# Optimization experiments

Measured on AMD Instinct MI355X. Metric: run time of the kernel, lower is better.

## Reference

```python
import jax, jax.numpy as jnp
import numpy as np

N = 50000      # nodes
E = 800000     # edges (before self-loops)
C_IN, C_H, C_OUT = 128, 64, 64
NEG_SLOPE = 0.2  # PyG GATConv default LeakyReLU slope


def setup_inputs() -> dict:
    key = jax.random.key(0)
    ks = jax.random.split(key, 16)
    def w(k, shape, fan_in):
        return jax.random.normal(k, shape, jnp.float32) / np.sqrt(fan_in)
    return {
        "x": jax.random.normal(ks[0], (N, C_IN), jnp.float32),
        "edge_index": jax.random.randint(ks[1], (2, E), 0, N, jnp.int32),
        "W1": w(ks[2], (C_IN, C_H), C_IN),
        "a_src1": w(ks[3], (C_H,), C_H),
        "a_dst1": w(ks[4], (C_H,), C_H),
        "b1": jnp.zeros((C_H,), jnp.float32),
        "W2": w(ks[5], (C_H, C_H), C_H),
        "a_src2": w(ks[6], (C_H,), C_H),
        "a_dst2": w(ks[7], (C_H,), C_H),
        "b2": jnp.zeros((C_H,), jnp.float32),
        "W3": w(ks[8], (C_H, C_OUT), C_H),
        "a_src3": w(ks[9], (C_OUT,), C_OUT),
        "a_dst3": w(ks[10], (C_OUT,), C_OUT),
        "b3": jnp.zeros((C_OUT,), jnp.float32),
    }


def _gat_conv(x, src, dst, W, a_src, a_dst, b):
    # Single-head GATConv (eval mode, self-loops already appended).
    h = x @ W                                   # [N, C]
    alpha_s = h @ a_src                         # [N]
    alpha_d = h @ a_dst                         # [N]
    e = jax.nn.leaky_relu(alpha_s[src] + alpha_d[dst], NEG_SLOPE)  # [E']
    # segment softmax over edges sharing the same destination node
    m = jax.lax.stop_gradient(jax.ops.segment_max(e, dst, num_segments=N))
    w = jnp.exp(e - m[dst])
    denom = jax.ops.segment_sum(w, dst, num_segments=N)
    alpha = w / denom[dst]                      # [E']
    out = jax.ops.segment_sum(h[src] * alpha[:, None], dst, num_segments=N)
    return out + b


def reference(x, edge_index, W1, a_src1, a_dst1, b1, W2, a_src2, a_dst2, b2,
              W3, a_src3, a_dst3, b3):
    loop = jnp.arange(N, dtype=edge_index.dtype)
    src = jnp.concatenate([edge_index[0], loop])  # add self-loops (PyG default)
    dst = jnp.concatenate([edge_index[1], loop])
    h = jax.nn.elu(_gat_conv(x, src, dst, W1, a_src1, a_dst1, b1))
    h = jax.nn.elu(_gat_conv(h, src, dst, W2, a_src2, a_dst2, b2))
    return _gat_conv(h, src, dst, W3, a_src3, a_dst3, b3)
```

## Files before the change

kernel.cpp:

```cpp
#include <hip/hip_runtime.h>
#include <hip/hip_bf16.h>
#include <math.h>

#define N_NODES 50000
#define N_EDGES 800000
#define ET_EDGES (N_EDGES + N_NODES)
#define NEG_SLOPE 0.2f
#define NBUCK ((N_NODES + 255) / 256)
#define CHUNK 4096
#define CAP   8192

typedef __hip_bfloat16 bf16;
typedef float f32x2 __attribute__((ext_vector_type(2)));

__device__ inline float bfbits(unsigned short u) {
    return __uint_as_float(((unsigned)u) << 16);
}
__device__ inline float bflo(unsigned u) { return __uint_as_float(u << 16); }
__device__ inline float bfhi(unsigned u) { return __uint_as_float(u & 0xffff0000u); }
__device__ inline f32x2 unpk(unsigned u) {
    f32x2 r; r.x = bflo(u); r.y = bfhi(u); return r;
}
__device__ inline f32x2 bcast2(float v) { f32x2 r; r.x = v; r.y = v; return r; }

struct PrepArgs {
    const void* src[12];
    float*      dst[12];
    int         n[12];
};

__global__ __launch_bounds__(256)
void prep(PrepArgs a, const unsigned short* __restrict__ w1raw,
          unsigned* __restrict__ flag, int* __restrict__ cur256)
{
    __shared__ unsigned sflag;
    const int tid = threadIdx.x;
    if (tid < 64) {
        float v0 = bfbits(w1raw[2 * tid]);
        float v1 = bfbits(w1raw[2 * tid + 1]);
        bool bad = !(fabsf(v0) <= 64.f && fabsf(v1) <= 64.f);
        unsigned long long b = __ballot(bad);
        if (tid == 0) sflag = (b == 0ull) ? 1u : 0u;
    }
    __syncthreads();
    const bool isbf = (sflag != 0u);
    const int which = blockIdx.y;

    if (which == 12) {
        int i = blockIdx.x * 256 + tid;
        if (i < NBUCK) cur256[i] = i * CAP;
        if (blockIdx.x == 0 && tid == 0) *flag = isbf ? 1u : 0u;
        return;
    }
    const int n = a.n[which];
    const void* s = a.src[which];
    float* d = a.dst[which];
    for (int i = blockIdx.x * 256 + tid; i < n; i += 8 * 256)
        d[i] = isbf ? bfbits(((const unsigned short*)s)[i])
                    : ((const float*)s)[i];
}

__global__ __launch_bounds__(256)
void binpass(const int* __restrict__ ei, int* __restrict__ cur256,
             unsigned* __restrict__ scratch)
{
    __shared__ int hist[NBUCK];
    __shared__ int lpre[NBUCK + 1];
    __shared__ int lcur[NBUCK];
    __shared__ int gbase[NBUCK];
    __shared__ int scan_a[256];
    __shared__ unsigned entry[CHUNK];

    const int tid = threadIdx.x;
    const int e0  = blockIdx.x * CHUNK;
    const int n   = min(CHUNK, ET_EDGES - e0);

    if (tid < NBUCK) hist[tid] = 0;
    __syncthreads();

    for (int k = tid; k < n; k += 256) {
        int e = e0 + k;
        int d = (e < N_EDGES) ? ei[N_EDGES + e] : e - N_EDGES;
        atomicAdd(&hist[d >> 8], 1);
    }
    __syncthreads();

    int v = (tid < NBUCK) ? hist[tid] : 0;
    scan_a[tid] = v;
    __syncthreads();
    for (int off = 1; off < 256; off <<= 1) {
        int t = (tid >= off) ? scan_a[tid - off] : 0;
        __syncthreads();
        scan_a[tid] += t;
        __syncthreads();
    }
    if (tid < NBUCK) lpre[tid] = scan_a[tid] - v;
    if (tid == NBUCK - 1) lpre[NBUCK] = scan_a[tid];
    if (tid < NBUCK) {
        gbase[tid] = v ? atomicAdd(&cur256[tid], v) : 0;
        lcur[tid] = 0;
    }
    __syncthreads();

    for (int k = tid; k < n; k += 256) {
        int e = e0 + k;
        int s, d;
        if (e < N_EDGES) { s = ei[e]; d = ei[N_EDGES + e]; }
        else             { s = d = e - N_EDGES; }
        int b = d >> 8;
        int p = atomicAdd(&lcur[b], 1);
        entry[lpre[b] + p] = ((unsigned)s << 8) | (unsigned)(d & 255);
    }
    __syncthreads();

    for (int i = tid; i < n; i += 256) {
        int lo = 0, hi = NBUCK;
        while (hi - lo > 1) {
            int mid = (lo + hi) >> 1;
            if (lpre[mid] <= i) lo = mid; else hi = mid;
        }
        scratch[gbase[lo] + (i - lpre[lo])] = entry[i];
    }
}

__global__ __launch_bounds__(256)
void fine_scatter(const int* __restrict__ cur256,
                  const unsigned* __restrict__ scratch,
                  int* __restrict__ csr_src,
                  int* __restrict__ rowptr)
{
    __shared__ int scnt[256];
    __shared__ int cnt[256];
    __shared__ int pre[256];
    const int tid = threadIdx.x;
    const int b   = blockIdx.x;
    const int nb  = b * 256;
    const int nn  = min(256, N_NODES - nb);

    int bv = (tid < NBUCK) ? (cur256[tid] - tid * CAP) : 0;
    scnt[tid] = bv;
    __syncthreads();
    for (int off = 1; off < 256; off <<= 1) {
        int u = (tid >= off) ? scnt[tid - off] : 0;
        __syncthreads();
        scnt[tid] += u;
        __syncthreads();
    }
    const int gb = scnt[b] - (cur256[b] - b * CAP);
    const int n  = cur256[b] - b * CAP;
    const long seg = (long)b * CAP;

    cnt[tid] = 0;
    __syncthreads();
    for (int i = tid; i < n; i += 256)
        atomicAdd(&cnt[scratch[seg + i] & 255u], 1);
    __syncthreads();

    int v = cnt[tid];
    pre[tid] = v;
    __syncthreads();
    for (int off = 1; off < 256; off <<= 1) {
        int t = (tid >= off) ? pre[tid - off] : 0;
        __syncthreads();
        pre[tid] += t;
        __syncthreads();
    }
    int excl = pre[tid] - v + gb;
    if (tid < nn) rowptr[nb + tid] = excl;
    if (b == NBUCK - 1 && tid == 0) rowptr[N_NODES] = ET_EDGES;
    cnt[tid] = excl;
    __syncthreads();

    for (int i = tid; i < n; i += 256) {
        unsigned e = scratch[seg + i];
        int p = atomicAdd(&cnt[e & 255u], 1);
        csr_src[p] = (int)(e >> 8);
    }
}

template<int CIN, int XMODE>
__global__ __launch_bounds__(256)
void gemm_alpha(const void* __restrict__ x,
                const float* __restrict__ W,
                const float* __restrict__ a_src,
                const float* __restrict__ a_dst,
                const unsigned* __restrict__ flag,
                bf16* __restrict__ hb,
                float* __restrict__ as_out,
                float* __restrict__ ad_out)
{
    constexpr int CINP = CIN + 4;
    __shared__ float sW[CIN * 64];
    __shared__ float sx[64 * CINP];
    const bool isbf = (XMODE == 2) || (XMODE == 1 && *flag != 0u);
    const int tid  = threadIdx.x;
    const int colg = tid & 15;
    const int rowg = tid >> 4;
    const int c0   = colg * 4;
    const int r0l  = rowg * 4;
    const int row0 = blockIdx.x * 64;

    for (int i = tid * 4; i < CIN * 64; i += 1024)
        *(float4*)&sW[i] = *(const float4*)&W[i];

    const long xbase = (long)row0 * CIN;
    const int  tile  = 64 * CIN;
    const int  limit = (N_NODES - row0) * CIN;
    if (isbf) {
        const unsigned short* xb = (const unsigned short*)x + xbase;
        for (int i = tid * 4; i < tile; i += 1024) {
            float4 v = {0.f, 0.f, 0.f, 0.f};
            if (i < limit) {
                ushort4 u = *(const ushort4*)&xb[i];
                v.x = bfbits(u.x); v.y = bfbits(u.y);
                v.z = bfbits(u.z); v.w = bfbits(u.w);
            }
            const int r = i / CIN, k = i & (CIN - 1);
            *(float4*)&sx[r * CINP + k] = v;
        }
    } else {
        const float* xf = (const float*)x + xbase;
        for (int i = tid * 4; i < tile; i += 1024) {
            float4 v = {0.f, 0.f, 0.f, 0.f};
            if (i < limit) v = *(const float4*)&xf[i];
            const int r = i / CIN, k = i & (CIN - 1);
            *(float4*)&sx[r * CINP + k] = v;
        }
    }
    __syncthreads();

    f32x2 acc[4][2];
#pragma unroll
    for (int r = 0; r < 4; ++r) {
        acc[r][0] = (f32x2){0.f, 0.f};
        acc[r][1] = (f32x2){0.f, 0.f};
    }

#pragma unroll 2
    for (int kk = 0; kk < CIN; kk += 4) {
        const float4 w0 = *(const float4*)&sW[(kk + 0) * 64 + c0];
        const float4 w1 = *(const float4*)&sW[(kk + 1) * 64 + c0];
        const float4 w2 = *(const float4*)&sW[(kk + 2) * 64 + c0];
        const float4 w3 = *(const float4*)&sW[(kk + 3) * 64 + c0];
        f32x2 w0lo; w0lo.x = w0.x; w0lo.y = w0.y;
        f32x2 w0hi; w0hi.x = w0.z; w0hi.y = w0.w;
        f32x2 w1lo; w1lo.x = w1.x; w1lo.y = w1.y;
        f32x2 w1hi; w1hi.x = w1.z; w1hi.y = w1.w;
        f32x2 w2lo; w2lo.x = w2.x; w2lo.y = w2.y;
        f32x2 w2hi; w2hi.x = w2.z; w2hi.y = w2.w;
        f32x2 w3lo; w3lo.x = w3.x; w3lo.y = w3.y;
        f32x2 w3hi; w3hi.x = w3.z; w3hi.y = w3.w;
#pragma unroll
        for (int r = 0; r < 4; ++r) {
            const float4 xv = *(const float4*)&sx[(r0l + r) * CINP + kk];
            acc[r][0] = __builtin_elementwise_fma(bcast2(xv.x), w0lo, acc[r][0]);
            acc[r][1] = __builtin_elementwise_fma(bcast2(xv.x), w0hi, acc[r][1]);
            acc[r][0] = __builtin_elementwise_fma(bcast2(xv.y), w1lo, acc[r][0]);
            acc[r][1] = __builtin_elementwise_fma(bcast2(xv.y), w1hi, acc[r][1]);
            acc[r][0] = __builtin_elementwise_fma(bcast2(xv.z), w2lo, acc[r][0]);
            acc[r][1] = __builtin_elementwise_fma(bcast2(xv.z), w2hi, acc[r][1]);
            acc[r][0] = __builtin_elementwise_fma(bcast2(xv.w), w3lo, acc[r][0]);
            acc[r][1] = __builtin_elementwise_fma(bcast2(xv.w), w3hi, acc[r][1]);
        }
    }

    const float4 sa4 = *(const float4*)&a_src[c0];
    const float4 sd4 = *(const float4*)&a_dst[c0];
#pragma unroll
    for (int r = 0; r < 4; ++r) {
        const int row = row0 + r0l + r;
        const float h0 = acc[r][0].x, h1 = acc[r][0].y;
        const float h2 = acc[r][1].x, h3 = acc[r][1].y;
        float vs = fmaf(h0, sa4.x, fmaf(h1, sa4.y, fmaf(h2, sa4.z, h3 * sa4.w)));
        float vd = fmaf(h0, sd4.x, fmaf(h1, sd4.y, fmaf(h2, sd4.z, h3 * sd4.w)));
#pragma unroll
        for (int off = 1; off < 16; off <<= 1) {
            vs += __shfl_xor(vs, off, 64);
            vd += __shfl_xor(vd, off, 64);
        }
        if (row < N_NODES) {
            uint2 u;
            u.x = ((unsigned)__bfloat16_as_ushort(__float2bfloat16(h0))) |
                  (((unsigned)__bfloat16_as_ushort(__float2bfloat16(h1))) << 16);
            u.y = ((unsigned)__bfloat16_as_ushort(__float2bfloat16(h2))) |
                  (((unsigned)__bfloat16_as_ushort(__float2bfloat16(h3))) << 16);
            *(uint2*)&((unsigned short*)hb)[(long)row * 64 + c0] = u;
            if (colg == 0) { as_out[row] = vs; ad_out[row] = vd; }
        }
    }
}

#define EDGE4_FMA(wX, pX) {                                                  \
    f32x2 w2_ = { wX, wX };                                                  \
    A0 = __builtin_elementwise_fma(w2_, unpk(pX.x), A0);                     \
    A1 = __builtin_elementwise_fma(w2_, unpk(pX.y), A1);                     \
    A2 = __builtin_elementwise_fma(w2_, unpk(pX.z), A2);                     \
    A3 = __builtin_elementwise_fma(w2_, unpk(pX.w), A3); }

template<bool DO_ELU, int OMODE>
__global__ __launch_bounds__(256)
void gat_gather(const int* __restrict__ rowptr,
                const int* __restrict__ csr_src,
                const float* __restrict__ as_in,
                const float* __restrict__ ad_in,
                const unsigned short* __restrict__ hb_in,
                const float* __restrict__ bias,
                void* __restrict__ out,
                const unsigned* __restrict__ flag)
{
    const int tid  = threadIdx.x;
    const int lane = tid & 63;
    const int l16  = lane & 15;
    const int gb16 = lane & 48;
    const int sub  = l16 >> 3;
    const int c8   = (l16 & 7) * 8;
    const int node = blockIdx.x * 16 + (tid >> 4);
    if (node >= N_NODES) return;

    const int beg = rowptr[node];
    const int deg = rowptr[node + 1] - beg;
    const float adv = ad_in[node];

    int   msrc0 = 0, msrc1 = 0;
    float mw0 = 0.f, mw1 = 0.f;
    if (l16 < deg) {
        msrc0 = csr_src[beg + l16];
        float v = as_in[msrc0] + adv;
        v = (v > 0.f) ? v : NEG_SLOPE * v;
        mw0 = __expf(fminf(v, 60.f));
    }
    if (16 + l16 < deg) {
        msrc1 = csr_src[beg + 16 + l16];
        float v = as_in[msrc1] + adv;
        v = (v > 0.f) ? v : NEG_SLOPE * v;
        mw1 = __expf(fminf(v, 60.f));
    }

    f32x2 A0 = {0.f, 0.f}, A1 = {0.f, 0.f}, A2 = {0.f, 0.f}, A3 = {0.f, 0.f};
    float dsum = 0.f;
    const int lim = (deg < 32) ? deg : 32;

#pragma unroll
    for (int j0 = 0; j0 < 16; j0 += 8) {
        if (j0 >= lim) break;
        const int jA = j0 + sub,     jB = j0 + 2 + sub;
        const int jC = j0 + 4 + sub, jD = j0 + 6 + sub;
        float wA = __shfl(mw0,   gb16 + jA, 64);
        int   sA = __shfl(msrc0, gb16 + jA, 64);
        float wB = __shfl(mw0,   gb16 + jB, 64);
        int   sB = __shfl(msrc0, gb16 + jB, 64);
        float wC = __shfl(mw0,   gb16 + jC, 64);
        int   sC = __shfl(msrc0, gb16 + jC, 64);
        float wD = __shfl(mw0,   gb16 + jD, 64);
        int   sD = __shfl(msrc0, gb16 + jD, 64);
        uint4 pA={0u,0u,0u,0u}, pB={0u,0u,0u,0u}, pC={0u,0u,0u,0u}, pD={0u,0u,0u,0u};
        const bool vA = jA < lim, vB = jB < lim, vC = jC < lim, vD = jD < lim;
        if (vA) pA = *(const uint4*)&hb_in[(long)sA * 64 + c8];
        if (vB) pB = *(const uint4*)&hb_in[(long)sB * 64 + c8];
        if (vC) pC = *(const uint4*)&hb_in[(long)sC * 64 + c8];
        if (vD) pD = *(const uint4*)&hb_in[(long)sD * 64 + c8];
        if (!vA) wA = 0.f;
        if (!vB) wB = 0.f;
        if (!vC) wC = 0.f;
        if (!vD) wD = 0.f;
        EDGE4_FMA(wA, pA) EDGE4_FMA(wB, pB) EDGE4_FMA(wC, pC) EDGE4_FMA(wD, pD)
        dsum += (wA + wB) + (wC + wD);
    }
#pragma unroll
    for (int j0 = 16; j0 < 32; j0 += 8) {
        if (j0 >= lim) break;
        const int jA = j0 + sub,     jB = j0 + 2 + sub;
        const int jC = j0 + 4 + sub, jD = j0 + 6 + sub;
        float wA = __shfl(mw1,   gb16 + jA - 16, 64);
        int   sA = __shfl(msrc1, gb16 + jA - 16, 64);
        float wB = __shfl(mw1,   gb16 + jB - 16, 64);
        int   sB = __shfl(msrc1, gb16 + jB - 16, 64);
        float wC = __shfl(mw1,   gb16 + jC - 16, 64);
        int   sC = __shfl(msrc1, gb16 + jC - 16, 64);
        float wD = __shfl(mw1,   gb16 + jD - 16, 64);
        int   sD = __shfl(msrc1, gb16 + jD - 16, 64);
        uint4 pA={0u,0u,0u,0u}, pB={0u,0u,0u,0u}, pC={0u,0u,0u,0u}, pD={0u,0u,0u,0u};
        const bool vA = jA < lim, vB = jB < lim, vC = jC < lim, vD = jD < lim;
        if (vA) pA = *(const uint4*)&hb_in[(long)sA * 64 + c8];
        if (vB) pB = *(const uint4*)&hb_in[(long)sB * 64 + c8];
        if (vC) pC = *(const uint4*)&hb_in[(long)sC * 64 + c8];
        if (vD) pD = *(const uint4*)&hb_in[(long)sD * 64 + c8];
        if (!vA) wA = 0.f;
        if (!vB) wB = 0.f;
        if (!vC) wC = 0.f;
        if (!vD) wD = 0.f;
        EDGE4_FMA(wA, pA) EDGE4_FMA(wB, pB) EDGE4_FMA(wC, pC) EDGE4_FMA(wD, pD)
        dsum += (wA + wB) + (wC + wD);
    }
    for (int j0 = 32; j0 < deg; j0 += 2) {
        const int j = j0 + sub;
        if (j < deg) {
            int sj = csr_src[beg + j];
            float v = as_in[sj] + adv;
            v = (v > 0.f) ? v : NEG_SLOPE * v;
            float wj = __expf(fminf(v, 60.f));
            const uint4 p = *(const uint4*)&hb_in[(long)sj * 64 + c8];
            EDGE4_FMA(wj, p)
            dsum += wj;
        }
    }

    float a0 = A0.x, a1 = A0.y, a2 = A1.x, a3 = A1.y;
    float a4 = A2.x, a5 = A2.y, a6 = A3.x, a7 = A3.y;
    a0 += __shfl_xor(a0, 8, 64); a1 += __shfl_xor(a1, 8, 64);
    a2 += __shfl_xor(a2, 8, 64); a3 += __shfl_xor(a3, 8, 64);
    a4 += __shfl_xor(a4, 8, 64); a5 += __shfl_xor(a5, 8, 64);
    a6 += __shfl_xor(a6, 8, 64); a7 += __shfl_xor(a7, 8, 64);
    dsum += __shfl_xor(dsum, 8, 64);

    if (sub == 0) {
        float inv = 1.f / dsum;
        float r[8] = {a0, a1, a2, a3, a4, a5, a6, a7};
#pragma unroll
        for (int k = 0; k < 8; ++k) {
            r[k] = r[k] * inv + bias[c8 + k];
            if (DO_ELU) r[k] = (r[k] > 0.f) ? r[k] : expm1f(r[k]);
        }
        long o = (long)node * 64 + c8;
        bool bfst = (OMODE == 0) || (*flag != 0u);
        if (bfst) {
            uint4 u;
            u.x = ((unsigned)__bfloat16_as_ushort(__float2bfloat16(r[0]))) |
                  (((unsigned)__bfloat16_as_ushort(__float2bfloat16(r[1]))) << 16);
            u.y = ((unsigned)__bfloat16_as_ushort(__float2bfloat16(r[2]))) |
                  (((unsigned)__bfloat16_as_ushort(__float2bfloat16(r[3]))) << 16);
            u.z = ((unsigned)__bfloat16_as_ushort(__float2bfloat16(r[4]))) |
                  (((unsigned)__bfloat16_as_ushort(__float2bfloat16(r[5]))) << 16);
            u.w = ((unsigned)__bfloat16_as_ushort(__float2bfloat16(r[6]))) |
                  (((unsigned)__bfloat16_as_ushort(__float2bfloat16(r[7]))) << 16);
            *(uint4*)&((unsigned short*)out)[o] = u;
        } else {
            float4 f0 = {r[0], r[1], r[2], r[3]};
            float4 f1 = {r[4], r[5], r[6], r[7]};
            *(float4*)&((float*)out)[o]     = f0;
            *(float4*)&((float*)out)[o + 4] = f1;
        }
    }
}

extern "C" void kernel_launch(void* const* d_in, const int* in_sizes, int n_in,
                              void* d_out, int out_size, void* d_ws, size_t ws_size,
                              hipStream_t stream)
{
    const void* x  = d_in[0];
    const int*  ei = (const int*)d_in[1];
    const void* pW1 = d_in[2],  *pas1 = d_in[3],  *pad1 = d_in[4],  *pb1 = d_in[5];
    const void* pW2 = d_in[6],  *pas2 = d_in[7],  *pad2 = d_in[8],  *pb2 = d_in[9];
    const void* pW3 = d_in[10], *pas3 = d_in[11], *pad3 = d_in[12], *pb3 = d_in[13];

    float* ws = (float*)d_ws;
    bf16*     hbA    = (bf16*)ws;
    bf16*     hbB    = (bf16*)(ws + (long)N_NODES * 32);
    float*    as_    = ws + (long)N_NODES * 64;
    float*    ad_    = as_ + N_NODES;
    int*      cur256 = (int*)(ad_ + N_NODES);
    int*      rowptr = cur256 + NBUCK;
    int*      csr_src= rowptr + N_NODES + 1;
    unsigned* scratch= (unsigned*)(csr_src + ET_EDGES);
    float*    prm    = (float*)(scratch + (long)NBUCK * CAP);
    unsigned* flag   = (unsigned*)(prm + 20000);

    float* W1 = prm;     float* as1 = W1 + 8192; float* ad1 = as1 + 64; float* b1 = ad1 + 64;
    float* W2 = b1 + 64; float* as2 = W2 + 4096; float* ad2 = as2 + 64; float* b2 = ad2 + 64;
    float* W3 = b2 + 64; float* as3 = W3 + 4096; float* ad3 = as3 + 64; float* b3 = ad3 + 64;

    PrepArgs pa;
    const void* srcs[12] = {pW1, pas1, pad1, pb1, pW2, pas2, pad2, pb2, pW3, pas3, pad3, pb3};
    float*      dsts[12] = {W1, as1, ad1, b1, W2, as2, ad2, b2, W3, as3, ad3, b3};
    int         ns[12]   = {8192, 64, 64, 64, 4096, 64, 64, 64, 4096, 64, 64, 64};
    for (int i = 0; i < 12; ++i) { pa.src[i] = srcs[i]; pa.dst[i] = dsts[i]; pa.n[i] = ns[i]; }
    prep<<<dim3(8, 13), 256, 0, stream>>>(pa, (const unsigned short*)pW1, flag, cur256);

    const int chunk_grid = (ET_EDGES + CHUNK - 1) / CHUNK;
    binpass<<<chunk_grid, 256, 0, stream>>>(ei, cur256, scratch);
    fine_scatter<<<NBUCK, 256, 0, stream>>>(cur256, scratch, csr_src, rowptr);

    const int gemm_grid = (N_NODES + 63) / 64;
    const int gat_grid  = (N_NODES + 15) / 16;

    gemm_alpha<128, 1><<<gemm_grid, 256, 0, stream>>>(
        x, W1, as1, ad1, flag, hbA, as_, ad_);
    gat_gather<true, 0><<<gat_grid, 256, 0, stream>>>(
        rowptr, csr_src, as_, ad_, (const unsigned short*)hbA, b1, hbB, flag);

    gemm_alpha<64, 2><<<gemm_grid, 256, 0, stream>>>(
        hbB, W2, as2, ad2, flag, hbA, as_, ad_);
    gat_gather<true, 0><<<gat_grid, 256, 0, stream>>>(
        rowptr, csr_src, as_, ad_, (const unsigned short*)hbA, b2, hbB, flag);

    gemm_alpha<64, 2><<<gemm_grid, 256, 0, stream>>>(
        hbB, W3, as3, ad3, flag, hbA, as_, ad_);
    gat_gather<false, 1><<<gat_grid, 256, 0, stream>>>(
        rowptr, csr_src, as_, ad_, (const unsigned short*)hbA, b3, d_out, flag);
}
```

Before: 251.8 us.

## Precompute per-edge attention weights in a separate kernel before gather

Adds a csr_dst array built during the CSR scatter and a new edge_w kernel that computes the leaky-relu/exp attention weight for every edge in a flat, coalesced pass. The gather kernel then reads the precomputed weights and source indices directly instead of computing them per node with shuffles. It also simplifies the gather into one generic loop over degree. In exchange it adds three extra launches, extra global traffic for csr_dst and ew (~850K entries each layer), and drops the register/shuffle staging of indices.

Result: slower. 276.0 us (+9.6%).

```diff
diff --git a/kernel.cpp b/kernel.cpp
--- a/kernel.cpp
+++ b/kernel.cpp
@@ -127,6 +127,7 @@
 void fine_scatter(const int* __restrict__ cur256,
                   const unsigned* __restrict__ scratch,
                   int* __restrict__ csr_src,
+                  int* __restrict__ csr_dst,
                   int* __restrict__ rowptr)
 {
     __shared__ int scnt[256];
@@ -175,6 +176,120 @@
         unsigned e = scratch[seg + i];
         int p = atomicAdd(&cnt[e & 255u], 1);
         csr_src[p] = (int)(e >> 8);
+        csr_dst[p] = nb + (int)(e & 255u);
+    }
+}
+
+__global__ __launch_bounds__(256)
+void edge_w(const int* __restrict__ csr_src, const int* __restrict__ csr_dst,
+            const float* __restrict__ as_, const float* __restrict__ ad_,
+            float* __restrict__ ew)
+{
+    const int i = (blockIdx.x * 256 + threadIdx.x) * 4;
+    if (i >= ET_EDGES) return;
+    const int4 s4 = *(const int4*)&csr_src[i];
+    const int4 d4 = *(const int4*)&csr_dst[i];
+    float v0 = as_[s4.x] + ad_[d4.x];
+    float v1 = as_[s4.y] + ad_[d4.y];
+    float v2 = as_[s4.z] + ad_[d4.z];
+    float v3 = as_[s4.w] + ad_[d4.w];
+    v0 = (v0 > 0.f) ? v0 : NEG_SLOPE * v0;
+    v1 = (v1 > 0.f) ? v1 : NEG_SLOPE * v1;
+    v2 = (v2 > 0.f) ? v2 : NEG_SLOPE * v2;
+    v3 = (v3 > 0.f) ? v3 : NEG_SLOPE * v3;
+    float4 w;
+    w.x = __expf(fminf(v0, 60.f));
+    w.y = __expf(fminf(v1, 60.f));
+    w.z = __expf(fminf(v2, 60.f));
+    w.w = __expf(fminf(v3, 60.f));
+    *(float4*)&ew[i] = w;
+}
+
+#define EDGE4_FMA(wX, pX) {                                                  \
+    f32x2 w2_ = { wX, wX };                                                  \
+    A0 = __builtin_elementwise_fma(w2_, unpk(pX.x), A0);                     \
+    A1 = __builtin_elementwise_fma(w2_, unpk(pX.y), A1);                     \
+    A2 = __builtin_elementwise_fma(w2_, unpk(pX.z), A2);                     \
+    A3 = __builtin_elementwise_fma(w2_, unpk(pX.w), A3); }
+
+template<bool DO_ELU, int OMODE>
+__global__ __launch_bounds__(256)
+void gat_gather(const int* __restrict__ rowptr,
+                const int* __restrict__ csr_src,
+                const float* __restrict__ ew,
+                const unsigned short* __restrict__ hb_in,
+                const float* __restrict__ bias,
+                void* __restrict__ out,
+                const unsigned* __restrict__ flag)
+{
+    const int tid  = threadIdx.x;
+    const int lane = tid & 63;
+    const int l16  = lane & 15;
+    const int sub  = l16 >> 3;
+    const int c8   = (l16 & 7) * 8;
+    const int node = blockIdx.x * 16 + (tid >> 4);
+    if (node >= N_NODES) return;
+
+    const int beg = rowptr[node];
+    const int deg = rowptr[node + 1] - beg;
+
+    f32x2 A0 = {0.f, 0.f}, A1 = {0.f, 0.f}, A2 = {0.f, 0.f}, A3 = {0.f, 0.f};
+    float dsum = 0.f;
+
+    for (int j0 = 0; j0 < deg; j0 += 8) {
+        const int jA = j0 + sub,     jB = j0 + 2 + sub;
+        const int jC = j0 + 4 + sub, jD = j0 + 6 + sub;
+        const bool vA = jA < deg, vB = jB < deg, vC = jC < deg, vD = jD < deg;
+        int sA = 0, sB = 0, sC = 0, sD = 0;
+        float wA = 0.f, wB = 0.f, wC = 0.f, wD = 0.f;
+        if (vA) { sA = csr_src[beg + jA]; wA = ew[beg + jA]; }
+        if (vB) { sB = csr_src[beg + jB]; wB = ew[beg + jB]; }
+        if (vC) { sC = csr_src[beg + jC]; wC = ew[beg + jC]; }
+        if (vD) { sD = csr_src[beg + jD]; wD = ew[beg + jD]; }
+        uint4 pA={0u,0u,0u,0u}, pB={0u,0u,0u,0u}, pC={0u,0u,0u,0u}, pD={0u,0u,0u,0u};
+        if (vA) pA = *(const uint4*)&hb_in[(long)sA * 64 + c8];
+        if (vB) pB = *(const uint4*)&hb_in[(long)sB * 64 + c8];
+        if (vC) pC = *(const uint4*)&hb_in[(long)sC * 64 + c8];
+        if (vD) pD = *(const uint4*)&hb_in[(long)sD * 64 + c8];
+        EDGE4_FMA(wA, pA) EDGE4_FMA(wB, pB) EDGE4_FMA(wC, pC) EDGE4_FMA(wD, pD)
+        dsum += (wA + wB) + (wC + wD);
+    }
+
+    float a0 = A0.x, a1 = A0.y, a2 = A1.x, a3 = A1.y;
+    float a4 = A2.x, a5 = A2.y, a6 = A3.x, a7 = A3.y;
+    a0 += __shfl_xor(a0, 8, 64); a1 += __shfl_xor(a1, 8, 64);
+    a2 += __shfl_xor(a2, 8, 64); a3 += __shfl_xor(a3, 8, 64);
+    a4 += __shfl_xor(a4, 8, 64); a5 += __shfl_xor(a5, 8, 64);
+    a6 += __shfl_xor(a6, 8, 64); a7 += __shfl_xor(a7, 8, 64);
+    dsum += __shfl_xor(dsum, 8, 64);
+
+    if (sub == 0) {
+        float inv = 1.f / dsum;
+        float r[8] = {a0, a1, a2, a3, a4, a5, a6, a7};
+#pragma unroll
+        for (int k = 0; k < 8; ++k) {
+            r[k] = r[k] * inv + bias[c8 + k];
+            if (DO_ELU) r[k] = (r[k] > 0.f) ? r[k] : expm1f(r[k]);
+        }
+        long o = (long)node * 64 + c8;
+        bool bfst = (OMODE == 0) || (*flag != 0u);
+        if (bfst) {
+            uint4 u;
+            u.x = ((unsigned)__bfloat16_as_ushort(__float2bfloat16(r[0]))) |
+                  (((unsigned)__bfloat16_as_ushort(__float2bfloat16(r[1]))) << 16);
+            u.y = ((unsigned)__bfloat16_as_ushort(__float2bfloat16(r[2]))) |
+                  (((unsigned)__bfloat16_as_ushort(__float2bfloat16(r[3]))) << 16);
+            u.z = ((unsigned)__bfloat16_as_ushort(__float2bfloat16(r[4]))) |
+                  (((unsigned)__bfloat16_as_ushort(__float2bfloat16(r[5]))) << 16);
+            u.w = ((unsigned)__bfloat16_as_ushort(__float2bfloat16(r[6]))) |
+                  (((unsigned)__bfloat16_as_ushort(__float2bfloat16(r[7]))) << 16);
+            *(uint4*)&((unsigned short*)out)[o] = u;
+        } else {
+            float4 f0 = {r[0], r[1], r[2], r[3]};
+            float4 f1 = {r[4], r[5], r[6], r[7]};
+            *(float4*)&((float*)out)[o]     = f0;
+            *(float4*)&((float*)out)[o + 4] = f1;
+        }
     }
 }
 
@@ -290,159 +405,6 @@
     }
 }
 
-#define EDGE4_FMA(wX, pX) {                                                  \
-    f32x2 w2_ = { wX, wX };                                                  \
-    A0 = __builtin_elementwise_fma(w2_, unpk(pX.x), A0);                     \
-    A1 = __builtin_elementwise_fma(w2_, unpk(pX.y), A1);                     \
-    A2 = __builtin_elementwise_fma(w2_, unpk(pX.z), A2);                     \
-    A3 = __builtin_elementwise_fma(w2_, unpk(pX.w), A3); }
-
-template<bool DO_ELU, int OMODE>
-__global__ __launch_bounds__(256)
-void gat_gather(const int* __restrict__ rowptr,
-                const int* __restrict__ csr_src,
-                const float* __restrict__ as_in,
-                const float* __restrict__ ad_in,
-                const unsigned short* __restrict__ hb_in,
-                const float* __restrict__ bias,
-                void* __restrict__ out,
-                const unsigned* __restrict__ flag)
-{
-    const int tid  = threadIdx.x;
-    const int lane = tid & 63;
-    const int l16  = lane & 15;
-    const int gb16 = lane & 48;
-    const int sub  = l16 >> 3;
-    const int c8   = (l16 & 7) * 8;
-    const int node = blockIdx.x * 16 + (tid >> 4);
-    if (node >= N_NODES) return;
-
-    const int beg = rowptr[node];
-    const int deg = rowptr[node + 1] - beg;
-    const float adv = ad_in[node];
-
-    int   msrc0 = 0, msrc1 = 0;
-    float mw0 = 0.f, mw1 = 0.f;
-    if (l16 < deg) {
-        msrc0 = csr_src[beg + l16];
-        float v = as_in[msrc0] + adv;
-        v = (v > 0.f) ? v : NEG_SLOPE * v;
-        mw0 = __expf(fminf(v, 60.f));
-    }
-    if (16 + l16 < deg) {
-        msrc1 = csr_src[beg + 16 + l16];
-        float v = as_in[msrc1] + adv;
-        v = (v > 0.f) ? v : NEG_SLOPE * v;
-        mw1 = __expf(fminf(v, 60.f));
-    }
-
-    f32x2 A0 = {0.f, 0.f}, A1 = {0.f, 0.f}, A2 = {0.f, 0.f}, A3 = {0.f, 0.f};
-    float dsum = 0.f;
-    const int lim = (deg < 32) ? deg : 32;
-
-#pragma unroll
-    for (int j0 = 0; j0 < 16; j0 += 8) {
-        if (j0 >= lim) break;
-        const int jA = j0 + sub,     jB = j0 + 2 + sub;
-        const int jC = j0 + 4 + sub, jD = j0 + 6 + sub;
-        float wA = __shfl(mw0,   gb16 + jA, 64);
-        int   sA = __shfl(msrc0, gb16 + jA, 64);
-        float wB = __shfl(mw0,   gb16 + jB, 64);
-        int   sB = __shfl(msrc0, gb16 + jB, 64);
-        float wC = __shfl(mw0,   gb16 + jC, 64);
-        int   sC = __shfl(msrc0, gb16 + jC, 64);
-        float wD = __shfl(mw0,   gb16 + jD, 64);
-        int   sD = __shfl(msrc0, gb16 + jD, 64);
-        uint4 pA={0u,0u,0u,0u}, pB={0u,0u,0u,0u}, pC={0u,0u,0u,0u}, pD={0u,0u,0u,0u};
-        const bool vA = jA < lim, vB = jB < lim, vC = jC < lim, vD = jD < lim;
-        if (vA) pA = *(const uint4*)&hb_in[(long)sA * 64 + c8];
-        if (vB) pB = *(const uint4*)&hb_in[(long)sB * 64 + c8];
-        if (vC) pC = *(const uint4*)&hb_in[(long)sC * 64 + c8];
-        if (vD) pD = *(const uint4*)&hb_in[(long)sD * 64 + c8];
-        if (!vA) wA = 0.f;
-        if (!vB) wB = 0.f;
-        if (!vC) wC = 0.f;
-        if (!vD) wD = 0.f;
-        EDGE4_FMA(wA, pA) EDGE4_FMA(wB, pB) EDGE4_FMA(wC, pC) EDGE4_FMA(wD, pD)
-        dsum += (wA + wB) + (wC + wD);
-    }
-#pragma unroll
-    for (int j0 = 16; j0 < 32; j0 += 8) {
-        if (j0 >= lim) break;
-        const int jA = j0 + sub,     jB = j0 + 2 + sub;
-        const int jC = j0 + 4 + sub, jD = j0 + 6 + sub;
-        float wA = __shfl(mw1,   gb16 + jA - 16, 64);
-        int   sA = __shfl(msrc1, gb16 + jA - 16, 64);
-        float wB = __shfl(mw1,   gb16 + jB - 16, 64);
-        int   sB = __shfl(msrc1, gb16 + jB - 16, 64);
-        float wC = __shfl(mw1,   gb16 + jC - 16, 64);
-        int   sC = __shfl(msrc1, gb16 + jC - 16, 64);
-        float wD = __shfl(mw1,   gb16 + jD - 16, 64);
-        int   sD = __shfl(msrc1, gb16 + jD - 16, 64);
-        uint4 pA={0u,0u,0u,0u}, pB={0u,0u,0u,0u}, pC={0u,0u,0u,0u}, pD={0u,0u,0u,0u};
-        const bool vA = jA < lim, vB = jB < lim, vC = jC < lim, vD = jD < lim;
-        if (vA) pA = *(const uint4*)&hb_in[(long)sA * 64 + c8];
-        if (vB) pB = *(const uint4*)&hb_in[(long)sB * 64 + c8];
-        if (vC) pC = *(const uint4*)&hb_in[(long)sC * 64 + c8];
-        if (vD) pD = *(const uint4*)&hb_in[(long)sD * 64 + c8];
-        if (!vA) wA = 0.f;
-        if (!vB) wB = 0.f;
-        if (!vC) wC = 0.f;
-        if (!vD) wD = 0.f;
-        EDGE4_FMA(wA, pA) EDGE4_FMA(wB, pB) EDGE4_FMA(wC, pC) EDGE4_FMA(wD, pD)
-        dsum += (wA + wB) + (wC + wD);
-    }
-    for (int j0 = 32; j0 < deg; j0 += 2) {
-        const int j = j0 + sub;
-        if (j < deg) {
-            int sj = csr_src[beg + j];
-            float v = as_in[sj] + adv;
-            v = (v > 0.f) ? v : NEG_SLOPE * v;
-            float wj = __expf(fminf(v, 60.f));
-            const uint4 p = *(const uint4*)&hb_in[(long)sj * 64 + c8];
-            EDGE4_FMA(wj, p)
-            dsum += wj;
-        }
-    }
-
-    float a0 = A0.x, a1 = A0.y, a2 = A1.x, a3 = A1.y;
-    float a4 = A2.x, a5 = A2.y, a6 = A3.x, a7 = A3.y;
-    a0 += __shfl_xor(a0, 8, 64); a1 += __shfl_xor(a1, 8, 64);
-    a2 += __shfl_xor(a2, 8, 64); a3 += __shfl_xor(a3, 8, 64);
-    a4 += __shfl_xor(a4, 8, 64); a5 += __shfl_xor(a5, 8, 64);
-    a6 += __shfl_xor(a6, 8, 64); a7 += __shfl_xor(a7, 8, 64);
-    dsum += __shfl_xor(dsum, 8, 64);
-
-    if (sub == 0) {
-        float inv = 1.f / dsum;
-        float r[8] = {a0, a1, a2, a3, a4, a5, a6, a7};
-#pragma unroll
-        for (int k = 0; k < 8; ++k) {
-            r[k] = r[k] * inv + bias[c8 + k];
-            if (DO_ELU) r[k] = (r[k] > 0.f) ? r[k] : expm1f(r[k]);
-        }
-        long o = (long)node * 64 + c8;
-        bool bfst = (OMODE == 0) || (*flag != 0u);
-        if (bfst) {
-            uint4 u;
-            u.x = ((unsigned)__bfloat16_as_ushort(__float2bfloat16(r[0]))) |
-                  (((unsigned)__bfloat16_as_ushort(__float2bfloat16(r[1]))) << 16);
-            u.y = ((unsigned)__bfloat16_as_ushort(__float2bfloat16(r[2]))) |
-                  (((unsigned)__bfloat16_as_ushort(__float2bfloat16(r[3]))) << 16);
-            u.z = ((unsigned)__bfloat16_as_ushort(__float2bfloat16(r[4]))) |
-                  (((unsigned)__bfloat16_as_ushort(__float2bfloat16(r[5]))) << 16);
-            u.w = ((unsigned)__bfloat16_as_ushort(__float2bfloat16(r[6]))) |
-                  (((unsigned)__bfloat16_as_ushort(__float2bfloat16(r[7]))) << 16);
-            *(uint4*)&((unsigned short*)out)[o] = u;
-        } else {
-            float4 f0 = {r[0], r[1], r[2], r[3]};
-            float4 f1 = {r[4], r[5], r[6], r[7]};
-            *(float4*)&((float*)out)[o]     = f0;
-            *(float4*)&((float*)out)[o + 4] = f1;
-        }
-    }
-}
-
 extern "C" void kernel_launch(void* const* d_in, const int* in_sizes, int n_in,
                               void* d_out, int out_size, void* d_ws, size_t ws_size,
                               hipStream_t stream)
@@ -461,8 +423,10 @@
     int*      cur256 = (int*)(ad_ + N_NODES);
     int*      rowptr = cur256 + NBUCK;
     int*      csr_src= rowptr + N_NODES + 1;
-    unsigned* scratch= (unsigned*)(csr_src + ET_EDGES);
-    float*    prm    = (float*)(scratch + (long)NBUCK * CAP);
+    int*      csr_dst= csr_src + ET_EDGES;
+    unsigned* scratch= (unsigned*)(csr_dst + ET_EDGES);
+    float*    ew     = (float*)(scratch + (long)NBUCK * CAP);
+    float*    prm    = ew + ET_EDGES;
     unsigned* flag   = (unsigned*)(prm + 20000);
 
     float* W1 = prm;     float* as1 = W1 + 8192; float* ad1 = as1 + 64; float* b1 = ad1 + 64;
@@ -478,23 +442,27 @@
 
     const int chunk_grid = (ET_EDGES + CHUNK - 1) / CHUNK;
     binpass<<<chunk_grid, 256, 0, stream>>>(ei, cur256, scratch);
-    fine_scatter<<<NBUCK, 256, 0, stream>>>(cur256, scratch, csr_src, rowptr);
+    fine_scatter<<<NBUCK, 256, 0, stream>>>(cur256, scratch, csr_src, csr_dst, rowptr);
 
     const int gemm_grid = (N_NODES + 63) / 64;
     const int gat_grid  = (N_NODES + 15) / 16;
+    const int ew_grid   = (ET_EDGES / 4 + 255) / 256;
 
     gemm_alpha<128, 1><<<gemm_grid, 256, 0, stream>>>(
         x, W1, as1, ad1, flag, hbA, as_, ad_);
+    edge_w<<<ew_grid, 256, 0, stream>>>(csr_src, csr_dst, as_, ad_, ew);
     gat_gather<true, 0><<<gat_grid, 256, 0, stream>>>(
-        rowptr, csr_src, as_, ad_, (const unsigned short*)hbA, b1, hbB, flag);
+        rowptr, csr_src, ew, (const unsigned short*)hbA, b1, hbB, flag);
 
     gemm_alpha<64, 2><<<gemm_grid, 256, 0, stream>>>(
         hbB, W2, as2, ad2, flag, hbA, as_, ad_);
+    edge_w<<<ew_grid, 256, 0, stream>>>(csr_src, csr_dst, as_, ad_, ew);
     gat_gather<true, 0><<<gat_grid, 256, 0, stream>>>(
-        rowptr, csr_src, as_, ad_, (const unsigned short*)hbA, b2, hbB, flag);
+        rowptr, csr_src, ew, (const unsigned short*)hbA, b2, hbB, flag);
 
     gemm_alpha<64, 2><<<gemm_grid, 256, 0, stream>>>(
         hbB, W3, as3, ad3, flag, hbA, as_, ad_);
+    edge_w<<<ew_grid, 256, 0, stream>>>(csr_src, csr_dst, as_, ad_, ew);
     gat_gather<false, 1><<<gat_grid, 256, 0, stream>>>(
-        rowptr, csr_src, as_, ad_, (const unsigned short*)hbA, b3, d_out, flag);
-}
+        rowptr, csr_src, ew, (const unsigned short*)hbA, b3, d_out, flag);
+}
```
